# Optimization experiments

Hardware: AMD Instinct MI355X
Metric: run time of the kernel (lower is better)

## Reference

```python
import jax, jax.numpy as jnp
import numpy as np

BLOCK_SIZE = 256


def setup_inputs() -> dict:
    key = jax.random.key(0)
    k1, k2, k3, k4 = jax.random.split(key, 4)
    B, T, C, H = 512, 256, 384, 64
    x = jax.random.normal(k1, (B, T, C), dtype=jnp.float32)
    Wk = jax.random.normal(k2, (H, C), dtype=jnp.float32) * (1.0 / np.sqrt(C))
    Wq = jax.random.normal(k3, (H, C), dtype=jnp.float32) * (1.0 / np.sqrt(C))
    Wv = jax.random.normal(k4, (H, C), dtype=jnp.float32) * (1.0 / np.sqrt(C))
    return {"x": x, "Wk": Wk, "Wq": Wq, "Wv": Wv}


def reference(x, Wk, Wq, Wv):
    # x: [B, T, C]; Wk/Wq/Wv: [H, C] (torch nn.Linear weight layout, bias=False)
    B, T, C = x.shape
    H = Wk.shape[0]
    k = jnp.einsum('btc,hc->bth', x, Wk)
    q = jnp.einsum('btc,hc->bth', x, Wq)
    v = jnp.einsum('btc,hc->bth', x, Wv)
    scale = 1.0 / jnp.sqrt(jnp.float32(H))
    scores = jnp.einsum('bqh,bkh->bqk', q, k) * scale  # [B, T, T]
    causal = jnp.tril(jnp.ones((T, T), dtype=bool))
    scores = jnp.where(causal, scores, -jnp.inf)
    weights = jax.nn.softmax(scores, axis=-1)
    # dropout is identity in eval mode
    out = jnp.einsum('bqk,bkh->bqh', weights, v)  # [B, T, H]
    return out
```

## Files before the change

### kernel.cpp

```cpp
#include <hip/hip_runtime.h>
#include <hip/hip_bf16.h>
#include <math.h>

#define TT 256
#define CC 384
#define HH 64

typedef float v4f   __attribute__((ext_vector_type(4)));
typedef short short8 __attribute__((ext_vector_type(8)));

#define MFMA(a, b, c) __builtin_amdgcn_mfma_f32_16x16x32_bf16((a), (b), (c), 0, 0, 0)

__device__ __forceinline__ unsigned short f2bf(float f) {
    unsigned int u = __float_as_uint(f);
    u += 0x7FFFu + ((u >> 16) & 1u);
    return (unsigned short)(u >> 16);
}

__device__ __forceinline__ ushort4 f2bf4(float4 f) {
    union { __hip_bfloat162 h2[2]; ushort4 u4; } cv;
    cv.h2[0] = __float22bfloat162_rn(make_float2(f.x, f.y));
    cv.h2[1] = __float22bfloat162_rn(make_float2(f.z, f.w));
    return cv.u4;
}

#define QSCALE 0.18033688f

__global__ __launch_bounds__(512, 4)
void qkv_proj(const float* __restrict__ x, const float* __restrict__ Wkp,
              const float* __restrict__ Wqp, const float* __restrict__ Wvp,
              unsigned short* __restrict__ qg, unsigned short* __restrict__ kg,
              unsigned short* __restrict__ vtg)
{
    __shared__ unsigned short sm[17408];
    unsigned short* x_s = sm;
    unsigned short* w_s = sm + 5120;
    unsigned short* epi = sm;

    const int tid  = threadIdx.x;
    const int wave = tid >> 6;
    const int lane = tid & 63;
    const int col  = lane & 15;
    const int quad = lane >> 4;
    const int row0 = blockIdx.x * 128;

    const int lr  = tid >> 3;
    const int lc4 = (tid & 7) * 4;

    const float* xp  = x   + (size_t)(row0 + lr) * CC + lc4;
    const float* wqp = Wqp + (size_t)lr * CC + lc4;
    const float* wkp = Wkp + (size_t)lr * CC + lc4;
    const float* wvp = Wvp + (size_t)lr * CC + lc4;

    v4f acc[12];
    #pragma unroll
    for (int j = 0; j < 12; ++j) acc[j] = (v4f){0.f, 0.f, 0.f, 0.f};

    float4 xA0 = *(const float4*)(xp);
    float4 xA1 = *(const float4*)(xp + 64 * CC);
    float4 wqA = *(const float4*)(wqp);
    float4 wkA = *(const float4*)(wkp);
    float4 wvA = *(const float4*)(wvp);

    const int afrag_off = (wave * 16 + col) * 40 + quad * 8;

    #pragma unroll
    for (int s = 0; s < 12; ++s) {
        float4 xB0, xB1, wqB, wkB, wvB;
        if (s < 11) {
            const int k0 = (s + 1) * 32;
            xB0 = *(const float4*)(xp + k0);
            xB1 = *(const float4*)(xp + 64 * CC + k0);
            wqB = *(const float4*)(wqp + k0);
            wkB = *(const float4*)(wkp + k0);
            wvB = *(const float4*)(wvp + k0);
        }
        __syncthreads();
        *(ushort4*)&x_s[lr * 40 + lc4]         = f2bf4(xA0);
        *(ushort4*)&x_s[(lr + 64) * 40 + lc4]  = f2bf4(xA1);
        *(ushort4*)&w_s[lr * 40 + lc4]         = f2bf4(wqA);
        *(ushort4*)&w_s[(64 + lr) * 40 + lc4]  = f2bf4(wkA);
        *(ushort4*)&w_s[(128 + lr) * 40 + lc4] = f2bf4(wvA);
        __syncthreads();
        const short8 a = *(const short8*)&x_s[afrag_off];
        #pragma unroll
        for (int nt = 0; nt < 12; ++nt) {
            const short8 bf = *(const short8*)&w_s[(nt * 16 + col) * 40 + quad * 8];
            acc[nt] = MFMA(a, bf, acc[nt]);
        }
        if (s < 11) { xA0 = xB0; xA1 = xB1; wqA = wqB; wkA = wkB; wvA = wvB; }
    }

    const int b    = row0 >> 8;
    const int half = (row0 >> 7) & 1;

    __syncthreads();
    #pragma unroll
    for (int nt = 0; nt < 8; ++nt) {
        #pragma unroll
        for (int r = 0; r < 4; ++r) {
            const int rl = wave * 16 + quad * 4 + r;
            const int n  = nt * 16 + col;
            float v = acc[nt][r];
            if (nt < 4) v *= QSCALE;
            epi[rl * 136 + n] = f2bf(v);
        }
    }
    __syncthreads();
    #pragma unroll
    for (int p = 0; p < 4; ++p) {
        const int idx = tid + p * 512;
        const int r = idx >> 4, ch = idx & 15;
        const short8 v = *(const short8*)&epi[r * 136 + ch * 8];
        const size_t base = (size_t)(row0 + r) * 64 + (ch & 7) * 8;
        if (ch < 8) *(short8*)&qg[base] = v;
        else        *(short8*)&kg[base] = v;
    }

    __syncthreads();
    #pragma unroll
    for (int nt = 8; nt < 12; ++nt) {
        #pragma unroll
        for (int r = 0; r < 4; ++r) {
            const int rl = wave * 16 + quad * 4 + r;
            const int h  = nt * 16 + col - 128;
            epi[h * 136 + rl] = f2bf(acc[nt][r]);
        }
    }
    __syncthreads();
    #pragma unroll
    for (int p = 0; p < 2; ++p) {
        const int idx = tid + p * 512;
        const int h = idx >> 4, ch = idx & 15;
        const short8 v = *(const short8*)&epi[h * 136 + ch * 8];
        *(short8*)&vtg[((size_t)b * 64 + h) * 256 + half * 128 + ch * 8] = v;
    }
}

__global__ __launch_bounds__(256, 4)
void attn(const unsigned short* __restrict__ qg, const unsigned short* __restrict__ kg,
          const unsigned short* __restrict__ vtg, float* __restrict__ out)
{
    __shared__ unsigned short Pb_all[4 * 16 * 40];
    const int tid  = threadIdx.x;
    const int wave = tid >> 6;
    const int lane = tid & 63;
    const int col  = lane & 15;
    const int quad = lane >> 4;
    const int b    = blockIdx.x >> 1;
    const int g    = blockIdx.x & 1;

    unsigned short* Pb = Pb_all + wave * 640;
    const unsigned short* kb_base = kg  + (size_t)b * 256 * 64;
    const unsigned short* vt_base = vtg + (size_t)b * 64 * 256;

    #pragma unroll
    for (int mi = 0; mi < 2; ++mi) {
        const int j  = g * 4 + wave;
        const int qt = mi ? (15 - j) : j;
        const size_t qoff = ((size_t)b * 256 + qt * 16 + col) * 64 + quad * 8;
        const short8 aq0 = *(const short8*)(qg + qoff);
        const short8 aq1 = *(const short8*)(qg + qoff + 32);

        float lsum[4];
        v4f oacc[4];
        #pragma unroll
        for (int r = 0; r < 4; ++r) lsum[r] = 0.f;
        #pragma unroll
        for (int hn = 0; hn < 4; ++hn) oacc[hn] = (v4f){0.f, 0.f, 0.f, 0.f};

        const int nch = qt / 2 + 1;
        short8 b00, b01, b10, b11;
        {
            const int ko0 = col * 64 + quad * 8;
            const int ko1 = (16 + col) * 64 + quad * 8;
            b00 = *(const short8*)(kb_base + ko0);
            b01 = *(const short8*)(kb_base + ko0 + 32);
            b10 = *(const short8*)(kb_base + ko1);
            b11 = *(const short8*)(kb_base + ko1 + 32);
        }
        for (int kc = 0; kc < nch; ++kc) {
            const int kb = kc * 32;
            v4f s0 = (v4f){0.f, 0.f, 0.f, 0.f};
            v4f s1 = (v4f){0.f, 0.f, 0.f, 0.f};
            s0 = MFMA(aq0, b00, s0);
            s0 = MFMA(aq1, b01, s0);
            s1 = MFMA(aq0, b10, s1);
            s1 = MFMA(aq1, b11, s1);
            if (kc + 1 < nch) {
                const int ko0 = (kb + 32 + col) * 64 + quad * 8;
                const int ko1 = (kb + 48 + col) * 64 + quad * 8;
                b00 = *(const short8*)(kb_base + ko0);
                b01 = *(const short8*)(kb_base + ko0 + 32);
                b10 = *(const short8*)(kb_base + ko1);
                b11 = *(const short8*)(kb_base + ko1 + 32);
            }
            const bool diag = (kc == qt / 2);
            #pragma unroll
            for (int r = 0; r < 4; ++r) {
                const int t = qt * 16 + quad * 4 + r;
                float v0 = s0[r];
                float v1 = s1[r];
                if (diag) {
                    if (kb + col > t)      v0 = -1e30f;
                    if (kb + 16 + col > t) v1 = -1e30f;
                }
                const float p0 = exp2f(v0);
                const float p1 = exp2f(v1);
                lsum[r] += p0 + p1;
                Pb[(quad * 4 + r) * 40 + col]      = f2bf(p0);
                Pb[(quad * 4 + r) * 40 + 16 + col] = f2bf(p1);
            }
            __threadfence_block();
            const short8 ap = *(const short8*)&Pb[col * 40 + quad * 8];
            #pragma unroll
            for (int hn = 0; hn < 4; ++hn) {
                const short8 bv = *(const short8*)(vt_base + (hn * 16 + col) * 256 + kb + quad * 8);
                oacc[hn] = MFMA(ap, bv, oacc[hn]);
            }
        }

        #pragma unroll
        for (int r = 0; r < 4; ++r) {
            float l = lsum[r];
            l += __shfl_xor(l, 1);
            l += __shfl_xor(l, 2);
            l += __shfl_xor(l, 4);
            l += __shfl_xor(l, 8);
            const int t = qt * 16 + quad * 4 + r;
            const float inv = 1.0f / l;
            float* op = out + ((size_t)b * TT + t) * HH;
            #pragma unroll
            for (int hn = 0; hn < 4; ++hn)
                op[hn * 16 + col] = oacc[hn][r] * inv;
        }
    }
}

extern "C" void kernel_launch(void* const* d_in, const int* in_sizes, int n_in,
                              void* d_out, int out_size, void* d_ws, size_t ws_size,
                              hipStream_t stream) {
    const float* x  = (const float*)d_in[0];
    const float* Wk = (const float*)d_in[1];
    const float* Wq = (const float*)d_in[2];
    const float* Wv = (const float*)d_in[3];
    float* out = (float*)d_out;

    unsigned short* qg  = (unsigned short*)d_ws;
    unsigned short* kg  = qg + (size_t)512 * 256 * 64;
    unsigned short* vtg = kg + (size_t)512 * 256 * 64;

    qkv_proj<<<dim3(1024), dim3(512), 0, stream>>>(x, Wk, Wq, Wv, qg, kg, vtg);
    attn<<<dim3(1024), dim3(256), 0, stream>>>(qg, kg, vtg, out);
}
```

Baseline: 335.8 us.

## Retile QKV projection waves into 2x4 grid of 64x48 output tiles

The projection kernel now assigns each of the 8 waves a 64-row by 48-column output tile (4x3 MFMA fragments) instead of a 16-row by 192-column strip. This cuts per-wave LDS fragment loads from 13 to 7 per k-step by reusing A and B fragments across more MFMAs. The global prefetch for the next k-step is moved after the LDS store barrier. The epilogue is rewritten to map the new tile layout onto the Q/K and transposed V staging buffers. The total accumulator register count stays the same.

```diff
diff --git a/kernel.cpp b/kernel.cpp
--- a/kernel.cpp
+++ b/kernel.cpp
@@ -44,6 +44,9 @@
     const int quad = lane >> 4;
     const int row0 = blockIdx.x * 128;
 
+    const int wr = wave >> 2;
+    const int wc = wave & 3;
+
     const int lr  = tid >> 3;
     const int lc4 = (tid & 7) * 4;
 
@@ -52,9 +55,11 @@
     const float* wkp = Wkp + (size_t)lr * CC + lc4;
     const float* wvp = Wvp + (size_t)lr * CC + lc4;
 
-    v4f acc[12];
-    #pragma unroll
-    for (int j = 0; j < 12; ++j) acc[j] = (v4f){0.f, 0.f, 0.f, 0.f};
+    v4f acc[4][3];
+    #pragma unroll
+    for (int m = 0; m < 4; ++m)
+        #pragma unroll
+        for (int n = 0; n < 3; ++n) acc[m][n] = (v4f){0.f, 0.f, 0.f, 0.f};
 
     float4 xA0 = *(const float4*)(xp);
     float4 xA1 = *(const float4*)(xp + 64 * CC);
@@ -62,10 +67,16 @@
     float4 wkA = *(const float4*)(wkp);
     float4 wvA = *(const float4*)(wvp);
 
-    const int afrag_off = (wave * 16 + col) * 40 + quad * 8;
-
     #pragma unroll
     for (int s = 0; s < 12; ++s) {
+        __syncthreads();
+        *(ushort4*)&x_s[lr * 40 + lc4]         = f2bf4(xA0);
+        *(ushort4*)&x_s[(lr + 64) * 40 + lc4]  = f2bf4(xA1);
+        *(ushort4*)&w_s[lr * 40 + lc4]         = f2bf4(wqA);
+        *(ushort4*)&w_s[(64 + lr) * 40 + lc4]  = f2bf4(wkA);
+        *(ushort4*)&w_s[(128 + lr) * 40 + lc4] = f2bf4(wvA);
+        __syncthreads();
+
         float4 xB0, xB1, wqB, wkB, wvB;
         if (s < 11) {
             const int k0 = (s + 1) * 32;
@@ -75,19 +86,20 @@
             wkB = *(const float4*)(wkp + k0);
             wvB = *(const float4*)(wvp + k0);
         }
-        __syncthreads();
-        *(ushort4*)&x_s[lr * 40 + lc4]         = f2bf4(xA0);
-        *(ushort4*)&x_s[(lr + 64) * 40 + lc4]  = f2bf4(xA1);
-        *(ushort4*)&w_s[lr * 40 + lc4]         = f2bf4(wqA);
-        *(ushort4*)&w_s[(64 + lr) * 40 + lc4]  = f2bf4(wkA);
-        *(ushort4*)&w_s[(128 + lr) * 40 + lc4] = f2bf4(wvA);
-        __syncthreads();
-        const short8 a = *(const short8*)&x_s[afrag_off];
-        #pragma unroll
-        for (int nt = 0; nt < 12; ++nt) {
-            const short8 bf = *(const short8*)&w_s[(nt * 16 + col) * 40 + quad * 8];
-            acc[nt] = MFMA(a, bf, acc[nt]);
-        }
+
+        short8 af[4], bf[3];
+        #pragma unroll
+        for (int m = 0; m < 4; ++m)
+            af[m] = *(const short8*)&x_s[(wr * 64 + m * 16 + col) * 40 + quad * 8];
+        #pragma unroll
+        for (int n = 0; n < 3; ++n)
+            bf[n] = *(const short8*)&w_s[(wc * 48 + n * 16 + col) * 40 + quad * 8];
+        #pragma unroll
+        for (int m = 0; m < 4; ++m)
+            #pragma unroll
+            for (int n = 0; n < 3; ++n)
+                acc[m][n] = MFMA(af[m], bf[n], acc[m][n]);
+
         if (s < 11) { xA0 = xB0; xA1 = xB1; wqA = wqB; wkA = wkB; wvA = wvB; }
     }
 
@@ -96,14 +108,19 @@
 
     __syncthreads();
     #pragma unroll
-    for (int nt = 0; nt < 8; ++nt) {
-        #pragma unroll
-        for (int r = 0; r < 4; ++r) {
-            const int rl = wave * 16 + quad * 4 + r;
-            const int n  = nt * 16 + col;
-            float v = acc[nt][r];
-            if (nt < 4) v *= QSCALE;
-            epi[rl * 136 + n] = f2bf(v);
+    for (int m = 0; m < 4; ++m) {
+        #pragma unroll
+        for (int n = 0; n < 3; ++n) {
+            const int gc = wc * 48 + n * 16;
+            if (gc < 128) {
+                #pragma unroll
+                for (int r = 0; r < 4; ++r) {
+                    const int rl = wr * 64 + m * 16 + quad * 4 + r;
+                    float v = acc[m][n][r];
+                    if (gc < 64) v *= QSCALE;
+                    epi[rl * 136 + gc + col] = f2bf(v);
+                }
+            }
         }
     }
     __syncthreads();
@@ -119,12 +136,18 @@
 
     __syncthreads();
     #pragma unroll
-    for (int nt = 8; nt < 12; ++nt) {
-        #pragma unroll
-        for (int r = 0; r < 4; ++r) {
-            const int rl = wave * 16 + quad * 4 + r;
-            const int h  = nt * 16 + col - 128;
-            epi[h * 136 + rl] = f2bf(acc[nt][r]);
+    for (int m = 0; m < 4; ++m) {
+        #pragma unroll
+        for (int n = 0; n < 3; ++n) {
+            const int gc = wc * 48 + n * 16;
+            if (gc >= 128) {
+                #pragma unroll
+                for (int r = 0; r < 4; ++r) {
+                    const int rl = wr * 64 + m * 16 + quad * 4 + r;
+                    const int h  = gc + col - 128;
+                    epi[h * 136 + rl] = f2bf(acc[m][n][r]);
+                }
+            }
         }
     }
     __syncthreads();
```

Result: slower. 350.3 us (+4.3%).
